# Kernel optimization log

Hardware: AMD Instinct MI355X
Metric: run time of the kernel (lower is better)

## Reference

```python
import jax, jax.numpy as jnp
from jax import lax
import numpy as np

DIM, DT_RANK, D_INNER, D_STATE = 256, 16, 256, 16

def _ssm_params(key, d, dt_rank, d_inner, n):
    k1, k2, k3 = jax.random.split(key, 3)
    Wdbc = jax.random.normal(k1, (d, dt_rank + 2 * n), jnp.float32) * 0.02
    Wdt = jax.random.normal(k2, (dt_rank, d_inner), jnp.float32) * 0.02
    bdt = jax.random.normal(k3, (d_inner,), jnp.float32) * 0.02
    Alog = jnp.log(jnp.tile(jnp.arange(1, n + 1, dtype=jnp.float32), (d_inner, 1)))
    D = jnp.ones((d_inner,), jnp.float32)
    return Wdbc, Wdt, bdt, Alog, D

def setup_inputs() -> dict:
    key = jax.random.key(0)
    ks = jax.random.split(key, 10)
    x = jax.random.normal(ks[0], (4, 4096, DIM), jnp.float32)
    ln_g = jnp.ones((DIM,), jnp.float32)
    ln_b = jnp.zeros((DIM,), jnp.float32)
    Wp = jax.random.normal(ks[1], (DIM, DIM), jnp.float32) * 0.02
    bp = jnp.zeros((DIM,), jnp.float32)
    Wcf = jax.random.normal(ks[2], (DIM, DIM), jnp.float32) * 0.02  # conv1d k=1 == pointwise matmul
    bcf = jnp.zeros((DIM,), jnp.float32)
    Wcb = jax.random.normal(ks[3], (DIM, DIM), jnp.float32) * 0.02
    bcb = jnp.zeros((DIM,), jnp.float32)
    Wdbc_f, Wdt_f, bdt_f, Alog_f, D_f = _ssm_params(ks[4], DIM, DT_RANK, D_INNER, D_STATE)
    Wdbc_b, Wdt_b, bdt_b, Alog_b, D_b = _ssm_params(ks[5], DIM, DT_RANK, D_INNER, D_STATE)
    return dict(x=x, ln_g=ln_g, ln_b=ln_b, Wp=Wp, bp=bp, Wcf=Wcf, bcf=bcf, Wcb=Wcb, bcb=bcb,
                Wdbc_f=Wdbc_f, Wdt_f=Wdt_f, bdt_f=bdt_f, Alog_f=Alog_f, D_f=D_f,
                Wdbc_b=Wdbc_b, Wdt_b=Wdt_b, bdt_b=bdt_b, Alog_b=Alog_b, D_b=D_b)

def _layernorm(x, g, b, eps=1e-5):
    mu = jnp.mean(x, -1, keepdims=True)
    var = jnp.var(x, -1, keepdims=True)
    return (x - mu) * lax.rsqrt(var + eps) * g + b

def _selective_scan(x, delta, A, B, C, D):
    # x, delta: [b,s,d]; A: [d,n]; B, C: [b,s,n]; D: [d]
    deltaA = jnp.exp(delta[..., None] * A)              # [b,s,d,n]
    BX = delta[..., None] * B[:, :, None, :] * x[..., None]  # [b,s,d,n]
    dA = jnp.moveaxis(deltaA, 1, 0)
    bx = jnp.moveaxis(BX, 1, 0)
    def step(h, inp):
        dA_t, bx_t = inp
        h = dA_t * h + bx_t
        return h, h
    h0 = jnp.zeros_like(dA[0])
    _, hs = lax.scan(step, h0, (dA, bx))                # [s,b,d,n]
    hs = jnp.moveaxis(hs, 0, 1)                          # [b,s,d,n]
    y = jnp.einsum('bsdn,bsn->bsd', hs, C) + D * x
    return y

def _ssm(x, Wdbc, Wdt, bdt, Alog, D):
    A = -jnp.exp(Alog)
    dbc = x @ Wdbc
    dt_r, B, C = jnp.split(dbc, [DT_RANK, DT_RANK + D_STATE], axis=-1)
    delta = jax.nn.softplus(dt_r @ Wdt + bdt)
    return _selective_scan(x, delta, A, B, C, D)

def _process(x, Wc, bc, Wdbc, Wdt, bdt, Alog, D):
    x = jax.nn.softplus(x @ Wc.T + bc)  # Conv1d k=1: out[e] = sum_d W[e,d] x[d] + b[e]
    return _ssm(x, Wdbc, Wdt, bdt, Alog, D)

def reference(x, ln_g, ln_b, Wp, bp, Wcf, bcf, Wcb, bcb,
              Wdbc_f, Wdt_f, bdt_f, Alog_f, D_f,
              Wdbc_b, Wdt_b, bdt_b, Alog_b, D_b):
    skip = x
    xn = _layernorm(x, ln_g, ln_b)
    z1 = xn @ Wp + bp  # proj used for both z1 and x (same layer twice)
    xp = z1
    x1 = jax.nn.silu(_process(xp, Wcf, bcf, Wdbc_f, Wdt_f, bdt_f, Alog_f, D_f))
    x2r = _process(jnp.flip(xp, 1), Wcb, bcb, Wdbc_b, Wdt_b, bdt_b, Alog_b, D_b)
    x2 = jax.nn.silu(jnp.flip(x2r, 1))
    z = jax.nn.silu(z1)
    return x1 * z + x2 * z + skip
```

## Files before the change

### kernel.cpp

```cpp
#include <hip/hip_runtime.h>
#include <math.h>

#define SB 4
#define SS 4096
#define SD 256
#define SN 16
#define ROWS 16
#define NRB 1024
#define NCH 128
#define CHL 32

#define BM 128
#define BN 64
#define BK 64
#define LDT 72

#define MBM 64
#define MLDZ 264
#define MLDT 72
#define MLDE 68

typedef __attribute__((ext_vector_type(8))) short bf16x8;
typedef __attribute__((ext_vector_type(4))) float f32x4;

__device__ __forceinline__ unsigned short f2bf(float f){
    unsigned int u = __float_as_uint(f);
    u += 0x7FFFu + ((u >> 16) & 1u);
    return (unsigned short)(u >> 16);
}
__device__ __forceinline__ float bf2f(unsigned short u){
    return __uint_as_float(((unsigned int)u) << 16);
}
__device__ __forceinline__ float softplus_f(float x){
    return fmaxf(x, 0.f) + __logf(1.f + __expf(-fabsf(x)));
}
__device__ __forceinline__ float silu_f(float x){
    return x * __builtin_amdgcn_rcpf(1.f + __expf(-x));
}

__global__ __launch_bounds__(256)
void k_prep(const float* __restrict__ Wp,
            const float* __restrict__ Wcf, const float* __restrict__ Wcb,
            const float* __restrict__ Wdbc0, const float* __restrict__ Wdt0,
            const float* __restrict__ Wdbc1, const float* __restrict__ Wdt1,
            unsigned short* __restrict__ WpT, unsigned short* __restrict__ Wc,
            unsigned short* __restrict__ G3W)
{
    int idx = blockIdx.x*256 + threadIdx.x;
    if (idx < 65536){
        int n = idx >> 8, k = idx & 255;
        WpT[idx] = f2bf(Wp[k*256 + n]);
    } else if (idx < 65536 + 131072){
        int j = idx - 65536;
        Wc[j] = f2bf(j < 65536 ? Wcf[j] : Wcb[j - 65536]);
    } else {
        int j = idx - 196608;
        int dir = j / 81920; int r = j - dir*81920;
        int n = r >> 8, d = r & 255;
        const float* Wdbc = dir ? Wdbc1 : Wdbc0;
        const float* Wdt  = dir ? Wdt1  : Wdt0;
        float v;
        if (n < 256){
            v = 0.f;
            #pragma unroll
            for (int q = 0; q < 16; ++q)
                v = fmaf(Wdbc[d*48 + q], Wdt[q*256 + n], v);
        } else if (n < 272) v = Wdbc[d*48 + 16 + (n-256)];
        else if (n < 288)   v = Wdbc[d*48 + 32 + (n-272)];
        else                v = 0.f;
        G3W[(size_t)dir*81920 + r] = f2bf(v);
    }
}

__global__ __launch_bounds__(256)
void k_ln(const float* __restrict__ x, const float* __restrict__ g,
          const float* __restrict__ bln, unsigned short* __restrict__ xnbf){
    int row0 = blockIdx.x * ROWS;
    int tid = threadIdx.x; int w = tid >> 6; int lane = tid & 63;
    #pragma unroll
    for (int rep = 0; rep < 4; ++rep){
        int j = rep*4 + w;
        const float* xr = x + (size_t)(row0 + j)*SD;
        float4 v = *(const float4*)(xr + lane*4);
        float s = v.x + v.y + v.z + v.w;
        #pragma unroll
        for (int off = 32; off; off >>= 1) s += __shfl_xor(s, off, 64);
        float mu = s * (1.f/256.f);
        float d0 = v.x-mu, d1 = v.y-mu, d2 = v.z-mu, d3 = v.w-mu;
        float q = d0*d0 + d1*d1 + d2*d2 + d3*d3;
        #pragma unroll
        for (int off = 32; off; off >>= 1) q += __shfl_xor(q, off, 64);
        float rstd = rsqrtf(q*(1.f/256.f) + 1e-5f);
        float4 gg = *(const float4*)(g + lane*4);
        float4 bb = *(const float4*)(bln + lane*4);
        ushort4 o;
        o.x = f2bf(d0*rstd*gg.x + bb.x);
        o.y = f2bf(d1*rstd*gg.y + bb.y);
        o.z = f2bf(d2*rstd*gg.z + bb.z);
        o.w = f2bf(d3*rstd*gg.w + bb.w);
        *(ushort4*)(xnbf + (size_t)(row0+j)*SD + lane*4) = o;
    }
}

__global__ __launch_bounds__(256, 5)
void k_gemm0(const unsigned short* __restrict__ A,
             const unsigned short* __restrict__ Bt,
             const float* __restrict__ bias0,
             unsigned short* __restrict__ obf)
{
    __shared__ unsigned short sMem[(BM + BN) * LDT];
    unsigned short (*sA)[LDT] = (unsigned short (*)[LDT])sMem;
    unsigned short (*sB)[LDT] = (unsigned short (*)[LDT])(sMem + BM*LDT);
    int ntile = blockIdx.x, mtile = blockIdx.y;
    int row0 = mtile * BM;
    int col0 = ntile * BN;

    int tid = threadIdx.x;
    uint4 ra[4], rb[2];
    auto gload = [&](int kt){
        int k0 = kt * BK;
        #pragma unroll
        for (int i = 0; i < 4; ++i){
            int idx = tid + i*256; int r = idx >> 3, kp = idx & 7;
            ra[i] = *(const uint4*)(A + (size_t)(row0 + r)*256 + k0 + kp*8);
        }
        #pragma unroll
        for (int i = 0; i < 2; ++i){
            int idx = tid + i*256; int r = idx >> 3, kp = idx & 7;
            rb[i] = *(const uint4*)(Bt + (size_t)(col0 + r)*256 + k0 + kp*8);
        }
    };
    auto swrite = [&](){
        #pragma unroll
        for (int i = 0; i < 4; ++i){
            int idx = tid + i*256; int r = idx >> 3, kp = idx & 7;
            *(uint4*)&sA[r][kp*8] = ra[i];
        }
        #pragma unroll
        for (int i = 0; i < 2; ++i){
            int idx = tid + i*256; int r = idx >> 3, kp = idx & 7;
            *(uint4*)&sB[r][kp*8] = rb[i];
        }
    };

    gload(0); swrite(); __syncthreads();

    int lane = tid & 63, w = tid >> 6;
    int wr = w >> 1, wc = w & 1;
    int lr = lane & 15, hi = lane >> 4;

    f32x4 acc[4][2];
    #pragma unroll
    for (int mf = 0; mf < 4; ++mf)
        #pragma unroll
        for (int nf = 0; nf < 2; ++nf)
            acc[mf][nf] = f32x4{0.f, 0.f, 0.f, 0.f};

    for (int kt = 0; kt < 4; ++kt){
        if (kt < 3) gload(kt + 1);
        #pragma unroll
        for (int kk = 0; kk < BK; kk += 32){
            bf16x8 af[4], bfr[2];
            #pragma unroll
            for (int mf = 0; mf < 4; ++mf)
                af[mf] = *(const bf16x8*)&sA[wr*64 + mf*16 + lr][kk + hi*8];
            #pragma unroll
            for (int nf = 0; nf < 2; ++nf)
                bfr[nf] = *(const bf16x8*)&sB[wc*32 + nf*16 + lr][kk + hi*8];
            #pragma unroll
            for (int mf = 0; mf < 4; ++mf)
                #pragma unroll
                for (int nf = 0; nf < 2; ++nf)
                    acc[mf][nf] = __builtin_amdgcn_mfma_f32_16x16x32_bf16(
                        af[mf], bfr[nf], acc[mf][nf], 0, 0, 0);
        }
        if (kt < 3){
            __syncthreads();
            swrite();
            __syncthreads();
        }
    }

    __syncthreads();
    unsigned short (*sOut)[LDT] = (unsigned short (*)[LDT])sMem;
    #pragma unroll
    for (int mf = 0; mf < 4; ++mf){
        #pragma unroll
        for (int nf = 0; nf < 2; ++nf){
            int col = col0 + wc*32 + nf*16 + lr;
            float bias = bias0[col];
            #pragma unroll
            for (int r = 0; r < 4; ++r)
                sOut[wr*64 + mf*16 + hi*4 + r][wc*32 + nf*16 + lr] =
                    f2bf(acc[mf][nf][r] + bias);
        }
    }
    __syncthreads();
    #pragma unroll
    for (int p = 0; p < 4; ++p){
        int chunk = tid + p*256;
        int r = chunk >> 3, cg = chunk & 7;
        uint4 v = *(const uint4*)&sOut[r][cg*8];
        *(uint4*)(obf + (size_t)(row0 + r)*256 + col0 + cg*8) = v;
    }
}

__global__ __launch_bounds__(256, 3)
void k_mid(const unsigned short* __restrict__ z1bf,
           const unsigned short* __restrict__ Wc,
           const unsigned short* __restrict__ G3W,
           const float* __restrict__ bc0, const float* __restrict__ bc1,
           const float* __restrict__ bdt0, const float* __restrict__ bdt1,
           unsigned short* __restrict__ xcbf,
           float* __restrict__ dg0, float* __restrict__ dg1,
           float* __restrict__ Bg0, float* __restrict__ Bg1,
           float* __restrict__ Cg0, float* __restrict__ Cg1)
{
    __shared__ unsigned short sZ[MBM*MLDZ];
    __shared__ unsigned short sX[MBM*MLDT];
    __shared__ unsigned short sBB[MBM*MLDT];
    int mtile = blockIdx.x, dir = blockIdx.y;
    int row0 = mtile*MBM;
    int tid = threadIdx.x;
    int lane = tid & 63, w = tid >> 6;
    int wr = w >> 1, wc = w & 1;
    int lr = lane & 15, hi = lane >> 4;

    {
        const uint4* src = (const uint4*)(z1bf + (size_t)row0*256);
        #pragma unroll
        for (int p = 0; p < 8; ++p){
            int idx = tid + p*256;
            int r = idx >> 5, cq = idx & 31;
            *(uint4*)&sZ[r*MLDZ + cq*8] = src[idx];
        }
    }
    __syncthreads();

    const float* bcp  = dir ? bc1  : bc0;
    const float* bdtp = dir ? bdt1 : bdt0;
    float* dgp = dir ? dg1 : dg0;
    const unsigned short* Gp = G3W + (size_t)dir*81920;

    f32x4 acc2[5][2][2];
    #pragma unroll
    for (int t5 = 0; t5 < 5; ++t5)
        #pragma unroll
        for (int mf = 0; mf < 2; ++mf)
            #pragma unroll
            for (int nf = 0; nf < 2; ++nf)
                acc2[t5][mf][nf] = f32x4{0.f,0.f,0.f,0.f};

    #pragma unroll 1
    for (int nt1 = 0; nt1 < 4; ++nt1){
        f32x4 acc1[2][2];
        #pragma unroll
        for (int mf = 0; mf < 2; ++mf)
            #pragma unroll
            for (int nf = 0; nf < 2; ++nf)
                acc1[mf][nf] = f32x4{0.f,0.f,0.f,0.f};
        for (int kt = 0; kt < 4; ++kt){
            #pragma unroll
            for (int p = 0; p < 2; ++p){
                int idx = tid + p*256; int r = idx>>3, c8 = idx&7;
                *(uint4*)&sBB[r*MLDT + c8*8] =
                    *(const uint4*)(Wc + (size_t)(dir*256 + nt1*64 + r)*256 + kt*64 + c8*8);
            }
            __syncthreads();
            #pragma unroll
            for (int kk = 0; kk < 64; kk += 32){
                bf16x8 af[2], bfr[2];
                af[0]  = *(const bf16x8*)&sZ[(wr*32 +      lr)*MLDZ + kt*64 + kk + hi*8];
                af[1]  = *(const bf16x8*)&sZ[(wr*32 + 16 + lr)*MLDZ + kt*64 + kk + hi*8];
                bfr[0] = *(const bf16x8*)&sBB[(wc*32 +      lr)*MLDT + kk + hi*8];
                bfr[1] = *(const bf16x8*)&sBB[(wc*32 + 16 + lr)*MLDT + kk + hi*8];
                #pragma unroll
                for (int mf = 0; mf < 2; ++mf)
                    #pragma unroll
                    for (int nf = 0; nf < 2; ++nf)
                        acc1[mf][nf] = __builtin_amdgcn_mfma_f32_16x16x32_bf16(
                            af[mf], bfr[nf], acc1[mf][nf], 0, 0, 0);
            }
            __syncthreads();
        }
        #pragma unroll
        for (int mf = 0; mf < 2; ++mf){
            #pragma unroll
            for (int nf = 0; nf < 2; ++nf){
                int colL = wc*32 + nf*16 + lr;
                float bias = bcp[nt1*64 + colL];
                #pragma unroll
                for (int r = 0; r < 4; ++r){
                    float v = softplus_f(acc1[mf][nf][r] + bias);
                    sX[(wr*32 + mf*16 + hi*4 + r)*MLDT + colL] = f2bf(v);
                }
            }
        }
        __syncthreads();
        #pragma unroll
        for (int p = 0; p < 2; ++p){
            int idx = tid + p*256; int r = idx>>3, c8 = idx&7;
            *(uint4*)(xcbf + (size_t)(row0 + r)*512 + dir*256 + nt1*64 + c8*8) =
                *(const uint4*)&sX[r*MLDT + c8*8];
        }
        #pragma unroll
        for (int nt2 = 0; nt2 < 5; ++nt2){
            __syncthreads();
            #pragma unroll
            for (int p = 0; p < 2; ++p){
                int idx = tid + p*256; int r = idx>>3, c8 = idx&7;
                *(uint4*)&sBB[r*MLDT + c8*8] =
                    *(const uint4*)(Gp + (size_t)(nt2*64 + r)*256 + nt1*64 + c8*8);
            }
            __syncthreads();
            #pragma unroll
            for (int kk = 0; kk < 64; kk += 32){
                bf16x8 af[2], bfr[2];
                af[0]  = *(const bf16x8*)&sX[(wr*32 +      lr)*MLDT + kk + hi*8];
                af[1]  = *(const bf16x8*)&sX[(wr*32 + 16 + lr)*MLDT + kk + hi*8];
                bfr[0] = *(const bf16x8*)&sBB[(wc*32 +      lr)*MLDT + kk + hi*8];
                bfr[1] = *(const bf16x8*)&sBB[(wc*32 + 16 + lr)*MLDT + kk + hi*8];
                #pragma unroll
                for (int mf = 0; mf < 2; ++mf)
                    #pragma unroll
                    for (int nf = 0; nf < 2; ++nf)
                        acc2[nt2][mf][nf] = __builtin_amdgcn_mfma_f32_16x16x32_bf16(
                            af[mf], bfr[nf], acc2[nt2][mf][nf], 0, 0, 0);
            }
        }
        __syncthreads();
    }

    float* sE = (float*)sZ;
    #pragma unroll
    for (int nt2 = 0; nt2 < 5; ++nt2){
        __syncthreads();
        #pragma unroll
        for (int mf = 0; mf < 2; ++mf)
            #pragma unroll
            for (int nf = 0; nf < 2; ++nf)
                #pragma unroll
                for (int r = 0; r < 4; ++r)
                    sE[(wr*32 + mf*16 + hi*4 + r)*MLDE + wc*32 + nf*16 + lr] =
                        acc2[nt2][mf][nf][r];
        __syncthreads();
        if (nt2 < 4){
            #pragma unroll
            for (int p = 0; p < 4; ++p){
                int idx = tid + p*256; int r = idx>>4, q = idx&15;
                float4 v = *(const float4*)&sE[r*MLDE + q*4];
                int col = nt2*64 + q*4;
                float4 bb = *(const float4*)(bdtp + col);
                v.x = softplus_f(v.x + bb.x);
                v.y = softplus_f(v.y + bb.y);
                v.z = softplus_f(v.z + bb.z);
                v.w = softplus_f(v.w + bb.w);
                *(float4*)(dgp + (size_t)(row0 + r)*SD + col) = v;
            }
        } else {
            float* Bp = dir ? Bg1 : Bg0;
            float* Cp = dir ? Cg1 : Cg0;
            int r = tid >> 2, q = tid & 3;
            float4 bv = *(const float4*)&sE[r*MLDE + q*4];
            float4 cv = *(const float4*)&sE[r*MLDE + 16 + q*4];
            *(float4*)(Bp + (size_t)(row0 + r)*SN + q*4) = bv;
            *(float4*)(Cp + (size_t)(row0 + r)*SN + q*4) = cv;
        }
    }
}

__global__ __launch_bounds__(256)
void k_scan_p1(const unsigned short* __restrict__ xcbf,
               const float* __restrict__ dg0, const float* __restrict__ B0, const float* __restrict__ Al0,
               const float* __restrict__ dg1, const float* __restrict__ B1, const float* __restrict__ Al1,
               float* __restrict__ hend, float* __restrict__ sdl)
{
    __shared__ float sB[CHL*SN];
    int blk = blockIdx.x;
    int c = blk & (NCH-1); int dir = (blk>>7) & 1; int b = blk>>8;
    const float* dg   = dir ? dg1 : dg0;
    const float* Bg   = dir ? B1  : B0;
    const float* Alog = dir ? Al1 : Al0;
    const unsigned short* xc = xcbf + dir*256;
    int d = threadIdx.x;
    #pragma unroll
    for (int k = 0; k < 2; ++k){
        int li = threadIdx.x + k*256;
        int i = li >> 4, n = li & 15;
        int tau = c*CHL + i;
        int t = dir ? (SS-1-tau) : tau;
        sB[li] = Bg[((size_t)b*SS + t)*SN + n];
    }
    float A[SN];
    #pragma unroll
    for (int k = 0; k < 4; ++k){
        float4 al = *(const float4*)(Alog + d*SN + k*4);
        A[k*4+0] = -__expf(al.x); A[k*4+1] = -__expf(al.y);
        A[k*4+2] = -__expf(al.z); A[k*4+3] = -__expf(al.w);
    }
    __syncthreads();
    int t0 = dir ? (SS-1 - c*CHL) : (c*CHL);
    const float* pd          = dg + ((size_t)b*SS + t0)*SD + d;
    const unsigned short* px = xc + ((size_t)b*SS + t0)*512 + d;
    int strided = dir ? -SD : SD;
    int stridex = dir ? -512 : 512;
    float h[SN];
    #pragma unroll
    for (int n = 0; n < SN; ++n) h[n] = 0.f;
    float sumdl = 0.f;
    float dl = *pd, xv = bf2f(*px);
    for (int i = 0; i < CHL; ++i){
        float dlN = 0.f, xvN = 0.f;
        if (i+1 < CHL){ pd += strided; px += stridex; dlN = *pd; xvN = bf2f(*px); }
        sumdl += dl;
        float dlx = dl * xv;
        const float4* b4 = (const float4*)&sB[i*SN];
        #pragma unroll
        for (int k = 0; k < 4; ++k){
            float4 bb = b4[k];
            h[k*4+0] = fmaf(__expf(dl*A[k*4+0]), h[k*4+0], bb.x*dlx);
            h[k*4+1] = fmaf(__expf(dl*A[k*4+1]), h[k*4+1], bb.y*dlx);
            h[k*4+2] = fmaf(__expf(dl*A[k*4+2]), h[k*4+2], bb.z*dlx);
            h[k*4+3] = fmaf(__expf(dl*A[k*4+3]), h[k*4+3], bb.w*dlx);
        }
        dl = dlN; xv = xvN;
    }
    size_t base = (((size_t)(b*2+dir)*NCH + c)*SD + d)*SN;
    #pragma unroll
    for (int k = 0; k < 4; ++k)
        *(float4*)(hend + base + k*4) = make_float4(h[k*4+0],h[k*4+1],h[k*4+2],h[k*4+3]);
    sdl[((size_t)(b*2+dir)*NCH + c)*SD + d] = sumdl;
}

__global__ __launch_bounds__(256)
void k_chain(const float* __restrict__ Al0, const float* __restrict__ Al1,
             float* hend, const float* __restrict__ sdl)
{
    int gidx = blockIdx.x*256 + threadIdx.x;
    int n = gidx & 15; int d = (gidx >> 4) & 255; int dirb = gidx >> 12;
    const float* Alog = (dirb & 1) ? Al1 : Al0;
    float A = -__expf(Alog[d*SN + n]);
    float H = 0.f;
    const size_t cs = (size_t)SD*SN;
    size_t idx  = (size_t)dirb*NCH*cs + (size_t)d*SN + n;
    size_t sidx = (size_t)dirb*NCH*SD + d;
    float he[4], sd[4];
    #pragma unroll
    for (int k = 0; k < 4; ++k){
        he[k] = hend[idx + (size_t)k*cs];
        sd[k] = sdl[sidx + (size_t)k*SD];
    }
    for (int cg = 0; cg < NCH; cg += 4){
        float heN[4] = {0.f,0.f,0.f,0.f};
        float sdN[4] = {0.f,0.f,0.f,0.f};
        if (cg + 4 < NCH){
            #pragma unroll
            for (int k = 0; k < 4; ++k){
                heN[k] = hend[idx + (size_t)(k+4)*cs];
                sdN[k] = sdl[sidx + (size_t)(k+4)*SD];
            }
        }
        #pragma unroll
        for (int k = 0; k < 4; ++k){
            hend[idx + (size_t)k*cs] = H;
            H = fmaf(__expf(A*sd[k]), H, he[k]);
        }
        #pragma unroll
        for (int k = 0; k < 4; ++k){ he[k] = heN[k]; sd[k] = sdN[k]; }
        idx += 4*cs; sidx += 4*SD;
    }
}

__global__ __launch_bounds__(256)
void k_scan_p2f(const unsigned short* __restrict__ xcbf,
                const float* __restrict__ dg0, const float* __restrict__ B0,
                const float* __restrict__ C0, const float* __restrict__ Al0,
                const float* __restrict__ Dv0,
                const float* __restrict__ dg1, const float* __restrict__ B1,
                const float* __restrict__ C1, const float* __restrict__ Al1,
                const float* __restrict__ Dv1,
                const float* __restrict__ hin,
                const unsigned short* __restrict__ z1bf,
                const float* __restrict__ x,
                float* __restrict__ out)
{
    __shared__ float yL[CHL*SD];
    __shared__ float sB0[CHL*SN], sC0[CHL*SN], sB1[CHL*SN], sC1[CHL*SN];
    int blk = blockIdx.x;
    int c = blk & (NCH-1); int b = blk >> 7;
    int d = threadIdx.x;
    #pragma unroll
    for (int k = 0; k < 2; ++k){
        int li = threadIdx.x + k*256;
        int i = li >> 4, n = li & 15;
        int tF = c*CHL + i;
        int tR = c*CHL + (CHL-1) - i;
        sB0[li] = B0[((size_t)b*SS + tF)*SN + n];
        sC0[li] = C0[((size_t)b*SS + tF)*SN + n];
        sB1[li] = B1[((size_t)b*SS + tR)*SN + n];
        sC1[li] = C1[((size_t)b*SS + tR)*SN + n];
    }
    __syncthreads();

    {
        float A[SN];
        #pragma unroll
        for (int k = 0; k < 4; ++k){
            float4 al = *(const float4*)(Al0 + d*SN + k*4);
            A[k*4+0] = -__expf(al.x); A[k*4+1] = -__expf(al.y);
            A[k*4+2] = -__expf(al.z); A[k*4+3] = -__expf(al.w);
        }
        float h[SN];
        size_t base = (((size_t)(b*2+0)*NCH + c)*SD + d)*SN;
        #pragma unroll
        for (int k = 0; k < 4; ++k){
            float4 hv = *(const float4*)(hin + base + k*4);
            h[k*4+0]=hv.x; h[k*4+1]=hv.y; h[k*4+2]=hv.z; h[k*4+3]=hv.w;
        }
        float Dd = Dv0[d];
        for (int i = 0; i < CHL; ++i){
            size_t rowb = (size_t)b*SS + c*CHL + i;
            float dl = dg0[rowb*SD + d];
            float xv = bf2f(xcbf[rowb*512 + d]);
            float dlx = dl * xv;
            float yv = Dd * xv;
            const float4* b4 = (const float4*)&sB0[i*SN];
            const float4* c4 = (const float4*)&sC0[i*SN];
            #pragma unroll
            for (int k = 0; k < 4; ++k){
                float4 bb = b4[k];
                float4 cc = c4[k];
                h[k*4+0] = fmaf(__expf(dl*A[k*4+0]), h[k*4+0], bb.x*dlx);
                yv = fmaf(h[k*4+0], cc.x, yv);
                h[k*4+1] = fmaf(__expf(dl*A[k*4+1]), h[k*4+1], bb.y*dlx);
                yv = fmaf(h[k*4+1], cc.y, yv);
                h[k*4+2] = fmaf(__expf(dl*A[k*4+2]), h[k*4+2], bb.z*dlx);
                yv = fmaf(h[k*4+2], cc.z, yv);
                h[k*4+3] = fmaf(__expf(dl*A[k*4+3]), h[k*4+3], bb.w*dlx);
                yv = fmaf(h[k*4+3], cc.w, yv);
            }
            yL[i*SD + d] = yv;
        }
    }
    {
        float A[SN];
        #pragma unroll
        for (int k = 0; k < 4; ++k){
            float4 al = *(const float4*)(Al1 + d*SN + k*4);
            A[k*4+0] = -__expf(al.x); A[k*4+1] = -__expf(al.y);
            A[k*4+2] = -__expf(al.z); A[k*4+3] = -__expf(al.w);
        }
        float h[SN];
        size_t base = (((size_t)(b*2+1)*NCH + (NCH-1-c))*SD + d)*SN;
        #pragma unroll
        for (int k = 0; k < 4; ++k){
            float4 hv = *(const float4*)(hin + base + k*4);
            h[k*4+0]=hv.x; h[k*4+1]=hv.y; h[k*4+2]=hv.z; h[k*4+3]=hv.w;
        }
        float Dd = Dv1[d];
        for (int ip = 0; ip < CHL; ++ip){
            int iloc = (CHL-1) - ip;
            size_t rowb = (size_t)b*SS + c*CHL + iloc;
            float dl = dg1[rowb*SD + d];
            float xv = bf2f(xcbf[rowb*512 + 256 + d]);
            float dlx = dl * xv;
            float yv = Dd * xv;
            const float4* b4 = (const float4*)&sB1[ip*SN];
            const float4* c4 = (const float4*)&sC1[ip*SN];
            #pragma unroll
            for (int k = 0; k < 4; ++k){
                float4 bb = b4[k];
                float4 cc = c4[k];
                h[k*4+0] = fmaf(__expf(dl*A[k*4+0]), h[k*4+0], bb.x*dlx);
                yv = fmaf(h[k*4+0], cc.x, yv);
                h[k*4+1] = fmaf(__expf(dl*A[k*4+1]), h[k*4+1], bb.y*dlx);
                yv = fmaf(h[k*4+1], cc.y, yv);
                h[k*4+2] = fmaf(__expf(dl*A[k*4+2]), h[k*4+2], bb.z*dlx);
                yv = fmaf(h[k*4+2], cc.z, yv);
                h[k*4+3] = fmaf(__expf(dl*A[k*4+3]), h[k*4+3], bb.w*dlx);
                yv = fmaf(h[k*4+3], cc.w, yv);
            }
            float y0v = yL[iloc*SD + d];
            float zv = bf2f(z1bf[rowb*SD + d]);
            float xo = x[rowb*SD + d];
            out[rowb*SD + d] = (silu_f(y0v) + silu_f(yv)) * silu_f(zv) + xo;
        }
    }
}

extern "C" void kernel_launch(void* const* d_in, const int* in_sizes, int n_in,
                              void* d_out, int out_size, void* d_ws, size_t ws_size,
                              hipStream_t stream) {
    const float* x     = (const float*)d_in[0];
    const float* ln_g  = (const float*)d_in[1];
    const float* ln_b  = (const float*)d_in[2];
    const float* Wp    = (const float*)d_in[3];
    const float* bp    = (const float*)d_in[4];
    const float* Wcf   = (const float*)d_in[5];
    const float* bcf   = (const float*)d_in[6];
    const float* Wcb   = (const float*)d_in[7];
    const float* bcb   = (const float*)d_in[8];
    const float* Wdbc_f= (const float*)d_in[9];
    const float* Wdt_f = (const float*)d_in[10];
    const float* bdt_f = (const float*)d_in[11];
    const float* Alog_f= (const float*)d_in[12];
    const float* D_f   = (const float*)d_in[13];
    const float* Wdbc_b= (const float*)d_in[14];
    const float* Wdt_b = (const float*)d_in[15];
    const float* bdt_b = (const float*)d_in[16];
    const float* Alog_b= (const float*)d_in[17];
    const float* D_b   = (const float*)d_in[18];
    float* out = (float*)d_out;

    float* ws = (float*)d_ws;
    const size_t NTOK  = (size_t)SB*SS;
    const size_t SZ_BD = NTOK*SD;
    const size_t SZ_BN = NTOK*SN;
    size_t off = 0;
    float* dg0   = ws + off; off += SZ_BD;
    float* dg1   = ws + off; off += SZ_BD;
    float* Bg0   = ws + off; off += SZ_BN;
    float* Bg1   = ws + off; off += SZ_BN;
    float* Cg0   = ws + off; off += SZ_BN;
    float* Cg1   = ws + off; off += SZ_BN;
    float* regA  = ws + off; off += SZ_BD;
    unsigned short* xnbf = (unsigned short*)regA;
    unsigned short* z1bf = xnbf + SZ_BD;
    float* regB  = ws + off; off += SZ_BD;
    unsigned short* xcbf = (unsigned short*)regB;
    float* hend  = ws + off; off += SZ_BD;
    float* sdl   = ws + off; off += (size_t)8*NCH*SD;
    unsigned short* WpT  = (unsigned short*)(ws + off); off += 65536/2;
    unsigned short* Wc   = (unsigned short*)(ws + off); off += 131072/2;
    unsigned short* G3W  = (unsigned short*)(ws + off); off += 163840/2;

    k_prep<<<1408, 256, 0, stream>>>(Wp, Wcf, Wcb, Wdbc_f, Wdt_f, Wdbc_b, Wdt_b,
                                     WpT, Wc, G3W);
    k_ln<<<NRB, 256, 0, stream>>>(x, ln_g, ln_b, xnbf);
    k_gemm0<<<dim3(4,128), 256, 0, stream>>>(xnbf, WpT, bp, z1bf);
    k_mid<<<dim3(256,2), 256, 0, stream>>>(z1bf, Wc, G3W,
        bcf, bcb, bdt_f, bdt_b, xcbf,
        dg0, dg1, Bg0, Bg1, Cg0, Cg1);
    k_scan_p1<<<1024, 256, 0, stream>>>(xcbf, dg0, Bg0, Alog_f,
                                        dg1, Bg1, Alog_b, hend, sdl);
    k_chain<<<128, 256, 0, stream>>>(Alog_f, Alog_b, hend, sdl);
    k_scan_p2f<<<512, 256, 0, stream>>>(xcbf,
        dg0, Bg0, Cg0, Alog_f, D_f,
        dg1, Bg1, Cg1, Alog_b, D_b,
        hend, z1bf, x, out);
}
```

Before: 161.5 us.

## Store delta in bf16 and feed MFMA B-operands directly from global memory

The delta tensors written by k_mid and read by both scan kernels are now stored as bf16 instead of fp32, halving that intermediate traffic. k_mid also drops the shared staging buffer for the weight tiles, loading Wc and G3W fragments straight from global memory into MFMA operands, which removes many __syncthreads. The sX A-fragments are hoisted out of the nt2 loop, and occupancy is lowered to 2 blocks per SM. Risks include reduced delta precision feeding exp in the scan, and uncoalesced or repeated global weight loads that depend on cache hits.

```diff
diff --git a/kernel.cpp b/kernel.cpp
--- a/kernel.cpp
+++ b/kernel.cpp
@@ -205,20 +205,19 @@
     }
 }
 
-__global__ __launch_bounds__(256, 3)
+__global__ __launch_bounds__(256, 2)
 void k_mid(const unsigned short* __restrict__ z1bf,
            const unsigned short* __restrict__ Wc,
            const unsigned short* __restrict__ G3W,
            const float* __restrict__ bc0, const float* __restrict__ bc1,
            const float* __restrict__ bdt0, const float* __restrict__ bdt1,
            unsigned short* __restrict__ xcbf,
-           float* __restrict__ dg0, float* __restrict__ dg1,
+           unsigned short* __restrict__ dg0, unsigned short* __restrict__ dg1,
            float* __restrict__ Bg0, float* __restrict__ Bg1,
            float* __restrict__ Cg0, float* __restrict__ Cg1)
 {
     __shared__ unsigned short sZ[MBM*MLDZ];
     __shared__ unsigned short sX[MBM*MLDT];
-    __shared__ unsigned short sBB[MBM*MLDT];
     int mtile = blockIdx.x, dir = blockIdx.y;
     int row0 = mtile*MBM;
     int tid = threadIdx.x;
@@ -239,8 +238,9 @@
 
     const float* bcp  = dir ? bc1  : bc0;
     const float* bdtp = dir ? bdt1 : bdt0;
-    float* dgp = dir ? dg1 : dg0;
-    const unsigned short* Gp = G3W + (size_t)dir*81920;
+    unsigned short* dgp = dir ? dg1 : dg0;
+    const unsigned short* Wcp = Wc + (size_t)dir*65536;
+    const unsigned short* Gp  = G3W + (size_t)dir*81920;
 
     f32x4 acc2[5][2][2];
     #pragma unroll
@@ -259,41 +259,32 @@
             #pragma unroll
             for (int nf = 0; nf < 2; ++nf)
                 acc1[mf][nf] = f32x4{0.f,0.f,0.f,0.f};
+        #pragma unroll
         for (int kt = 0; kt < 4; ++kt){
             #pragma unroll
-            for (int p = 0; p < 2; ++p){
-                int idx = tid + p*256; int r = idx>>3, c8 = idx&7;
-                *(uint4*)&sBB[r*MLDT + c8*8] =
-                    *(const uint4*)(Wc + (size_t)(dir*256 + nt1*64 + r)*256 + kt*64 + c8*8);
+            for (int kk = 0; kk < 64; kk += 32){
+                bf16x8 wf0 = *(const bf16x8*)(Wcp + (size_t)(nt1*64 + wc*32 +      lr)*256 + kt*64 + kk + hi*8);
+                bf16x8 wf1 = *(const bf16x8*)(Wcp + (size_t)(nt1*64 + wc*32 + 16 + lr)*256 + kt*64 + kk + hi*8);
+                bf16x8 zf0 = *(const bf16x8*)&sZ[(wr*32 +      lr)*MLDZ + kt*64 + kk + hi*8];
+                bf16x8 zf1 = *(const bf16x8*)&sZ[(wr*32 + 16 + lr)*MLDZ + kt*64 + kk + hi*8];
+                acc1[0][0] = __builtin_amdgcn_mfma_f32_16x16x32_bf16(wf0, zf0, acc1[0][0], 0,0,0);
+                acc1[0][1] = __builtin_amdgcn_mfma_f32_16x16x32_bf16(wf1, zf0, acc1[0][1], 0,0,0);
+                acc1[1][0] = __builtin_amdgcn_mfma_f32_16x16x32_bf16(wf0, zf1, acc1[1][0], 0,0,0);
+                acc1[1][1] = __builtin_amdgcn_mfma_f32_16x16x32_bf16(wf1, zf1, acc1[1][1], 0,0,0);
             }
-            __syncthreads();
-            #pragma unroll
-            for (int kk = 0; kk < 64; kk += 32){
-                bf16x8 af[2], bfr[2];
-                af[0]  = *(const bf16x8*)&sZ[(wr*32 +      lr)*MLDZ + kt*64 + kk + hi*8];
-                af[1]  = *(const bf16x8*)&sZ[(wr*32 + 16 + lr)*MLDZ + kt*64 + kk + hi*8];
-                bfr[0] = *(const bf16x8*)&sBB[(wc*32 +      lr)*MLDT + kk + hi*8];
-                bfr[1] = *(const bf16x8*)&sBB[(wc*32 + 16 + lr)*MLDT + kk + hi*8];
-                #pragma unroll
-                for (int mf = 0; mf < 2; ++mf)
-                    #pragma unroll
-                    for (int nf = 0; nf < 2; ++nf)
-                        acc1[mf][nf] = __builtin_amdgcn_mfma_f32_16x16x32_bf16(
-                            af[mf], bfr[nf], acc1[mf][nf], 0, 0, 0);
-            }
-            __syncthreads();
-        }
+        }
+        __syncthreads();
         #pragma unroll
         for (int mf = 0; mf < 2; ++mf){
             #pragma unroll
             for (int nf = 0; nf < 2; ++nf){
-                int colL = wc*32 + nf*16 + lr;
-                float bias = bcp[nt1*64 + colL];
-                #pragma unroll
-                for (int r = 0; r < 4; ++r){
-                    float v = softplus_f(acc1[mf][nf][r] + bias);
-                    sX[(wr*32 + mf*16 + hi*4 + r)*MLDT + colL] = f2bf(v);
-                }
+                float4 bb = *(const float4*)(bcp + nt1*64 + wc*32 + nf*16 + hi*4);
+                ushort4 o;
+                o.x = f2bf(softplus_f(acc1[mf][nf][0] + bb.x));
+                o.y = f2bf(softplus_f(acc1[mf][nf][1] + bb.y));
+                o.z = f2bf(softplus_f(acc1[mf][nf][2] + bb.z));
+                o.w = f2bf(softplus_f(acc1[mf][nf][3] + bb.w));
+                *(ushort4*)&sX[(wr*32 + mf*16 + lr)*MLDT + wc*32 + nf*16 + hi*4] = o;
             }
         }
         __syncthreads();
@@ -303,32 +294,24 @@
             *(uint4*)(xcbf + (size_t)(row0 + r)*512 + dir*256 + nt1*64 + c8*8) =
                 *(const uint4*)&sX[r*MLDT + c8*8];
         }
+        bf16x8 af[2][2];
+        #pragma unroll
+        for (int mf = 0; mf < 2; ++mf)
+            #pragma unroll
+            for (int k2 = 0; k2 < 2; ++k2)
+                af[mf][k2] = *(const bf16x8*)&sX[(wr*32 + mf*16 + lr)*MLDT + k2*32 + hi*8];
         #pragma unroll
         for (int nt2 = 0; nt2 < 5; ++nt2){
-            __syncthreads();
-            #pragma unroll
-            for (int p = 0; p < 2; ++p){
-                int idx = tid + p*256; int r = idx>>3, c8 = idx&7;
-                *(uint4*)&sBB[r*MLDT + c8*8] =
-                    *(const uint4*)(Gp + (size_t)(nt2*64 + r)*256 + nt1*64 + c8*8);
+            #pragma unroll
+            for (int k2 = 0; k2 < 2; ++k2){
+                bf16x8 gf0 = *(const bf16x8*)(Gp + (size_t)(nt2*64 + wc*32 +      lr)*256 + nt1*64 + k2*32 + hi*8);
+                bf16x8 gf1 = *(const bf16x8*)(Gp + (size_t)(nt2*64 + wc*32 + 16 + lr)*256 + nt1*64 + k2*32 + hi*8);
+                acc2[nt2][0][0] = __builtin_amdgcn_mfma_f32_16x16x32_bf16(af[0][k2], gf0, acc2[nt2][0][0], 0,0,0);
+                acc2[nt2][0][1] = __builtin_amdgcn_mfma_f32_16x16x32_bf16(af[0][k2], gf1, acc2[nt2][0][1], 0,0,0);
+                acc2[nt2][1][0] = __builtin_amdgcn_mfma_f32_16x16x32_bf16(af[1][k2], gf0, acc2[nt2][1][0], 0,0,0);
+                acc2[nt2][1][1] = __builtin_amdgcn_mfma_f32_16x16x32_bf16(af[1][k2], gf1, acc2[nt2][1][1], 0,0,0);
             }
-            __syncthreads();
-            #pragma unroll
-            for (int kk = 0; kk < 64; kk += 32){
-                bf16x8 af[2], bfr[2];
-                af[0]  = *(const bf16x8*)&sX[(wr*32 +      lr)*MLDT + kk + hi*8];
-                af[1]  = *(const bf16x8*)&sX[(wr*32 + 16 + lr)*MLDT + kk + hi*8];
-                bfr[0] = *(const bf16x8*)&sBB[(wc*32 +      lr)*MLDT + kk + hi*8];
-                bfr[1] = *(const bf16x8*)&sBB[(wc*32 + 16 + lr)*MLDT + kk + hi*8];
-                #pragma unroll
-                for (int mf = 0; mf < 2; ++mf)
-                    #pragma unroll
-                    for (int nf = 0; nf < 2; ++nf)
-                        acc2[nt2][mf][nf] = __builtin_amdgcn_mfma_f32_16x16x32_bf16(
-                            af[mf], bfr[nf], acc2[nt2][mf][nf], 0, 0, 0);
-            }
-        }
-        __syncthreads();
+        }
     }
 
     float* sE = (float*)sZ;
@@ -346,16 +329,24 @@
         __syncthreads();
         if (nt2 < 4){
             #pragma unroll
-            for (int p = 0; p < 4; ++p){
-                int idx = tid + p*256; int r = idx>>4, q = idx&15;
-                float4 v = *(const float4*)&sE[r*MLDE + q*4];
-                int col = nt2*64 + q*4;
-                float4 bb = *(const float4*)(bdtp + col);
-                v.x = softplus_f(v.x + bb.x);
-                v.y = softplus_f(v.y + bb.y);
-                v.z = softplus_f(v.z + bb.z);
-                v.w = softplus_f(v.w + bb.w);
-                *(float4*)(dgp + (size_t)(row0 + r)*SD + col) = v;
+            for (int p = 0; p < 2; ++p){
+                int idx = tid + p*256; int r = idx>>3, c8 = idx&7;
+                float4 v0 = *(const float4*)&sE[r*MLDE + c8*8];
+                float4 v1 = *(const float4*)&sE[r*MLDE + c8*8 + 4];
+                int col = nt2*64 + c8*8;
+                float4 b0 = *(const float4*)(bdtp + col);
+                float4 b1 = *(const float4*)(bdtp + col + 4);
+                ushort4 o0, o1;
+                o0.x = f2bf(softplus_f(v0.x + b0.x));
+                o0.y = f2bf(softplus_f(v0.y + b0.y));
+                o0.z = f2bf(softplus_f(v0.z + b0.z));
+                o0.w = f2bf(softplus_f(v0.w + b0.w));
+                o1.x = f2bf(softplus_f(v1.x + b1.x));
+                o1.y = f2bf(softplus_f(v1.y + b1.y));
+                o1.z = f2bf(softplus_f(v1.z + b1.z));
+                o1.w = f2bf(softplus_f(v1.w + b1.w));
+                ushort4 pk[2] = {o0, o1};
+                *(uint4*)(dgp + (size_t)(row0 + r)*SD + col) = *(const uint4*)pk;
             }
         } else {
             float* Bp = dir ? Bg1 : Bg0;
@@ -371,14 +362,14 @@
 
 __global__ __launch_bounds__(256)
 void k_scan_p1(const unsigned short* __restrict__ xcbf,
-               const float* __restrict__ dg0, const float* __restrict__ B0, const float* __restrict__ Al0,
-               const float* __restrict__ dg1, const float* __restrict__ B1, const float* __restrict__ Al1,
+               const unsigned short* __restrict__ dg0, const float* __restrict__ B0, const float* __restrict__ Al0,
+               const unsigned short* __restrict__ dg1, const float* __restrict__ B1, const float* __restrict__ Al1,
                float* __restrict__ hend, float* __restrict__ sdl)
 {
     __shared__ float sB[CHL*SN];
     int blk = blockIdx.x;
     int c = blk & (NCH-1); int dir = (blk>>7) & 1; int b = blk>>8;
-    const float* dg   = dir ? dg1 : dg0;
+    const unsigned short* dg = dir ? dg1 : dg0;
     const float* Bg   = dir ? B1  : B0;
     const float* Alog = dir ? Al1 : Al0;
     const unsigned short* xc = xcbf + dir*256;
@@ -400,7 +391,7 @@
     }
     __syncthreads();
     int t0 = dir ? (SS-1 - c*CHL) : (c*CHL);
-    const float* pd          = dg + ((size_t)b*SS + t0)*SD + d;
+    const unsigned short* pd = dg + ((size_t)b*SS + t0)*SD + d;
     const unsigned short* px = xc + ((size_t)b*SS + t0)*512 + d;
     int strided = dir ? -SD : SD;
     int stridex = dir ? -512 : 512;
@@ -408,10 +399,10 @@
     #pragma unroll
     for (int n = 0; n < SN; ++n) h[n] = 0.f;
     float sumdl = 0.f;
-    float dl = *pd, xv = bf2f(*px);
+    float dl = bf2f(*pd), xv = bf2f(*px);
     for (int i = 0; i < CHL; ++i){
         float dlN = 0.f, xvN = 0.f;
-        if (i+1 < CHL){ pd += strided; px += stridex; dlN = *pd; xvN = bf2f(*px); }
+        if (i+1 < CHL){ pd += strided; px += stridex; dlN = bf2f(*pd); xvN = bf2f(*px); }
         sumdl += dl;
         float dlx = dl * xv;
         const float4* b4 = (const float4*)&sB[i*SN];
@@ -473,10 +464,10 @@
 
 __global__ __launch_bounds__(256)
 void k_scan_p2f(const unsigned short* __restrict__ xcbf,
-                const float* __restrict__ dg0, const float* __restrict__ B0,
+                const unsigned short* __restrict__ dg0, const float* __restrict__ B0,
                 const float* __restrict__ C0, const float* __restrict__ Al0,
                 const float* __restrict__ Dv0,
-                const float* __restrict__ dg1, const float* __restrict__ B1,
+                const unsigned short* __restrict__ dg1, const float* __restrict__ B1,
                 const float* __restrict__ C1, const float* __restrict__ Al1,
                 const float* __restrict__ Dv1,
                 const float* __restrict__ hin,
@@ -520,7 +511,7 @@
         float Dd = Dv0[d];
         for (int i = 0; i < CHL; ++i){
             size_t rowb = (size_t)b*SS + c*CHL + i;
-            float dl = dg0[rowb*SD + d];
+            float dl = bf2f(dg0[rowb*SD + d]);
             float xv = bf2f(xcbf[rowb*512 + d]);
             float dlx = dl * xv;
             float yv = Dd * xv;
@@ -561,7 +552,7 @@
         for (int ip = 0; ip < CHL; ++ip){
             int iloc = (CHL-1) - ip;
             size_t rowb = (size_t)b*SS + c*CHL + iloc;
-            float dl = dg1[rowb*SD + d];
+            float dl = bf2f(dg1[rowb*SD + d]);
             float xv = bf2f(xcbf[rowb*512 + 256 + d]);
             float dlx = dl * xv;
             float yv = Dd * xv;
@@ -617,8 +608,9 @@
     const size_t SZ_BD = NTOK*SD;
     const size_t SZ_BN = NTOK*SN;
     size_t off = 0;
-    float* dg0   = ws + off; off += SZ_BD;
-    float* dg1   = ws + off; off += SZ_BD;
+    float* dgr   = ws + off; off += SZ_BD;
+    unsigned short* dg0 = (unsigned short*)dgr;
+    unsigned short* dg1 = dg0 + SZ_BD;
     float* Bg0   = ws + off; off += SZ_BN;
     float* Bg1   = ws + off; off += SZ_BN;
     float* Cg0   = ws + off; off += SZ_BN;
```

Measured after the change: 165.0 us. 1.02x slower.
